# Performance work log

Measured on AMD Instinct MI355X. Metric: run time of the kernel, lower is better.

## Reference

```python
import jax, jax.numpy as jnp
import numpy as np

D_ATT = 256
D_GROUP = 32
N_GROUP = D_ATT // D_GROUP


def setup_inputs() -> dict:
    key = jax.random.key(0)
    ks = jax.random.split(key, 6)
    B, L = 4, 512
    import math
    s = 1.0 / math.sqrt(D_ATT)
    return {
        "x": jax.random.normal(ks[0], (B, L, D_ATT), dtype=jnp.float32),
        "Wq": jax.random.normal(ks[1], (D_ATT, D_ATT), dtype=jnp.float32) * s * 0.06,
        "Wk": jax.random.normal(ks[2], (D_ATT, D_ATT), dtype=jnp.float32) * s * 0.06,
        "Wv": jax.random.normal(ks[3], (D_ATT, D_ATT), dtype=jnp.float32) * s * 0.06,
        "w_mlp": jax.random.normal(ks[4], (D_GROUP,), dtype=jnp.float32) * 0.1,
        "b_mlp": jax.random.normal(ks[5], (1,), dtype=jnp.float32) * 0.1,
    }


def reference(x, Wq, Wk, Wv, w_mlp, b_mlp):
    B, L, d_att = x.shape
    G, Dg = N_GROUP, D_GROUP
    # nn.Linear(bias=False): y = x @ W.T
    Q = x @ Wq.T  # (B, L, d_att)
    K = x @ Wk.T
    V = x @ Wv.T
    Qg = Q.reshape(B, L, 1, G, Dg)
    Kg = K.reshape(B, 1, L, G, Dg)
    # group_MLP: ReLU -> Linear(Dg, 1) -> ReLU, applied to Q-K diff
    # diff: (B, Lq, Lk, G, Dg) -- the huge intermediate a fused kernel would avoid
    diff = Qg - Kg
    attn = jnp.einsum('bqkgd,d->bqkg', jax.nn.relu(diff), w_mlp) + b_mlp[0]
    attn = jax.nn.relu(attn)
    # positional_adding_bias=0, positional_multiplying_bias=1 (defaults), no mask
    attn = jax.nn.softmax(attn, axis=2)  # softmax over key positions
    # NOTE: original views V as (B, L, d_group, n_group) -- asymmetric grouping, kept faithful
    Vg = V.reshape(B, L, Dg, G)
    out = jnp.einsum('bqkg,bkdg->bqdg', attn, Vg)  # (B, Lq, Dg, G)
    return out.reshape(B, L, d_att)
```

## Files before the change

kernel.cpp:

```cpp
#include <hip/hip_runtime.h>

typedef float f32x2 __attribute__((ext_vector_type(2)));
typedef float f32x4 __attribute__((ext_vector_type(4)));
typedef short bf16x8 __attribute__((ext_vector_type(8)));

#define LL 512
#define M_ROWS 2048
#define KC 768

__device__ __forceinline__ float quad_swap1(float x) {
    return __int_as_float(__builtin_amdgcn_mov_dpp(__float_as_int(x), 0xB1, 0xF, 0xF, true));
}
__device__ __forceinline__ float quad_swap2(float x) {
    return __int_as_float(__builtin_amdgcn_mov_dpp(__float_as_int(x), 0x4E, 0xF, 0xF, true));
}

__device__ __forceinline__ unsigned short bf16_rtne(float x) {
    unsigned u = __float_as_uint(x);
    return (unsigned short)((u + 0x7fffu + ((u >> 16) & 1u)) >> 16);
}
__device__ __forceinline__ float bf16_to_f(unsigned short h) {
    return __uint_as_float((unsigned)h << 16);
}

__global__ __launch_bounds__(64) void split_bf16(
    const float* __restrict__ X, const float* __restrict__ Wq,
    const float* __restrict__ Wk, const float* __restrict__ Wv,
    unsigned short* __restrict__ Xc, unsigned short* __restrict__ Wc)
{
    const int row = blockIdx.x;
    const int t = threadIdx.x;
    const float* src;
    unsigned short* hi1; unsigned short* hi2; unsigned short* lo1;
    if (row < M_ROWS) {
        src = X + (size_t)row * 256;
        hi1 = Xc + (size_t)row * KC;
        hi2 = hi1 + 256;
        lo1 = hi1 + 512;
    } else {
        const int n = row - M_ROWS;
        const int mat = n >> 8, c = n & 255;
        const int srow = (mat == 2) ? (((c & 31) << 3) | (c >> 5)) : c;
        src = (mat == 0 ? Wq : (mat == 1 ? Wk : Wv)) + (size_t)srow * 256;
        hi1 = Wc + (size_t)n * KC;
        lo1 = hi1 + 256;
        hi2 = hi1 + 512;
    }
    const f32x4 v = *(const f32x4*)(src + t * 4);
    ushort4 h, l;
    h.x = bf16_rtne(v.x); h.y = bf16_rtne(v.y); h.z = bf16_rtne(v.z); h.w = bf16_rtne(v.w);
    l.x = bf16_rtne(v.x - bf16_to_f(h.x));
    l.y = bf16_rtne(v.y - bf16_to_f(h.y));
    l.z = bf16_rtne(v.z - bf16_to_f(h.z));
    l.w = bf16_rtne(v.w - bf16_to_f(h.w));
    *(ushort4*)(hi1 + t * 4) = h;
    *(ushort4*)(hi2 + t * 4) = h;
    *(ushort4*)(lo1 + t * 4) = l;
}

__global__ __launch_bounds__(64) void qkv_mfma(
    const unsigned short* __restrict__ Xc, const unsigned short* __restrict__ Wc,
    float* __restrict__ Y)
{
    const int bid = blockIdx.x;
    const int m0 = (bid & 31) * 64;
    const int n0 = (bid >> 5) * 64;
    const int l = threadIdx.x;
    const int lr = l & 15;
    const int lk = (l >> 4) * 8;

    size_t aoff[4], boff[4];
#pragma unroll
    for (int i = 0; i < 4; ++i) {
        aoff[i] = (size_t)(m0 + i * 16 + lr) * KC + lk;
        boff[i] = (size_t)(n0 + i * 16 + lr) * KC + lk;
    }

    f32x4 acc[4][4];
#pragma unroll
    for (int i = 0; i < 4; ++i)
#pragma unroll
        for (int j = 0; j < 4; ++j) acc[i][j] = (f32x4){0.f, 0.f, 0.f, 0.f};

    bf16x8 A0[4], B0[4], A1[4], B1[4];
#pragma unroll
    for (int i = 0; i < 4; ++i) {
        A0[i] = *(const bf16x8*)(Xc + aoff[i]);
        B0[i] = *(const bf16x8*)(Wc + boff[i]);
    }

#pragma unroll 1
    for (int it = 0; it < 24; it += 2) {
        const int ks1 = (it + 1) * 32;
#pragma unroll
        for (int i = 0; i < 4; ++i) {
            A1[i] = *(const bf16x8*)(Xc + aoff[i] + ks1);
            B1[i] = *(const bf16x8*)(Wc + boff[i] + ks1);
        }
#pragma unroll
        for (int ai = 0; ai < 4; ++ai)
#pragma unroll
            for (int bi = 0; bi < 4; ++bi)
                acc[ai][bi] = __builtin_amdgcn_mfma_f32_16x16x32_bf16(
                    A0[ai], B0[bi], acc[ai][bi], 0, 0, 0);
        if (it + 2 < 24) {
            const int ks2 = (it + 2) * 32;
#pragma unroll
            for (int i = 0; i < 4; ++i) {
                A0[i] = *(const bf16x8*)(Xc + aoff[i] + ks2);
                B0[i] = *(const bf16x8*)(Wc + boff[i] + ks2);
            }
        }
#pragma unroll
        for (int ai = 0; ai < 4; ++ai)
#pragma unroll
            for (int bi = 0; bi < 4; ++bi)
                acc[ai][bi] = __builtin_amdgcn_mfma_f32_16x16x32_bf16(
                    A1[ai], B1[bi], acc[ai][bi], 0, 0, 0);
    }

    const int mat = n0 >> 8;
    float* Yb = Y + (size_t)mat * M_ROWS * 256;
#pragma unroll
    for (int ai = 0; ai < 4; ++ai)
#pragma unroll
        for (int bi = 0; bi < 4; ++bi) {
            const int col = (n0 & 255) + bi * 16 + lr;
#pragma unroll
            for (int r = 0; r < 4; ++r) {
                const int row = m0 + ai * 16 + (l >> 4) * 4 + r;
                Yb[(size_t)row * 256 + col] = acc[ai][bi][r];
            }
        }
}

#define ACC_S 73
__global__ __launch_bounds__(256, 1) void attn_fused(
    const float* __restrict__ Y,
    const float* __restrict__ w_mlp, const float* __restrict__ b_mlp,
    float* __restrict__ out)
{
    const float* Qm = Y;
    const float* Km = Y + (size_t)M_ROWS * 256;
    const float* Vt = Y + (size_t)2 * M_ROWS * 256;

    const int bid = blockIdx.x;
    const int b = bid & 3;
    const int q0 = (bid >> 2) * 8;

    const int t = threadIdx.x;
    const int dh = t & 3;
    const int g = (t >> 2) & 7;
    const int p = t >> 5;

    __shared__ float accbuf[8][32][ACC_S];
    __shared__ float ltot[8][8];

    const int doff = g * 32 + dh * 8;
    const float bias = b_mlp[0];

    f32x2 w2[4];
    {
        f32x4 wa = *(const f32x4*)(w_mlp + dh * 8);
        f32x4 wb = *(const f32x4*)(w_mlp + dh * 8 + 4);
        w2[0] = __builtin_shufflevector(wa, wa, 0, 1);
        w2[1] = __builtin_shufflevector(wa, wa, 2, 3);
        w2[2] = __builtin_shufflevector(wb, wb, 0, 1);
        w2[3] = __builtin_shufflevector(wb, wb, 2, 3);
    }

    f32x2 qr2[8][4];
#pragma unroll
    for (int q = 0; q < 8; ++q) {
        const float* qp = Qm + ((size_t)(b * LL) + q0 + q) * 256 + doff;
        f32x4 qa = *(const f32x4*)qp;
        f32x4 qb = *(const f32x4*)(qp + 4);
        qr2[q][0] = __builtin_shufflevector(qa, qa, 0, 1);
        qr2[q][1] = __builtin_shufflevector(qa, qa, 2, 3);
        qr2[q][2] = __builtin_shufflevector(qb, qb, 0, 1);
        qr2[q][3] = __builtin_shufflevector(qb, qb, 2, 3);
    }

    f32x2 acc2[8][4];
#pragma unroll
    for (int q = 0; q < 8; ++q)
#pragma unroll
        for (int j = 0; j < 4; ++j) acc2[q][j] = (f32x2){0.f, 0.f};
    float l[8] = {0.f, 0.f, 0.f, 0.f, 0.f, 0.f, 0.f, 0.f};

    const float* kptr = Km + ((size_t)(b * LL) + p) * 256 + doff;
    const float* vptr = Vt + ((size_t)(b * LL) + p) * 256 + doff;

    auto compute = [&](f32x4 ka, f32x4 kb, f32x4 va, f32x4 vb) {
        f32x2 k2[4] = {__builtin_shufflevector(ka, ka, 0, 1),
                       __builtin_shufflevector(ka, ka, 2, 3),
                       __builtin_shufflevector(kb, kb, 0, 1),
                       __builtin_shufflevector(kb, kb, 2, 3)};
        f32x2 v2[4] = {__builtin_shufflevector(va, va, 0, 1),
                       __builtin_shufflevector(va, va, 2, 3),
                       __builtin_shufflevector(vb, vb, 0, 1),
                       __builtin_shufflevector(vb, vb, 2, 3)};
        const f32x2 z2 = {0.f, 0.f};
#pragma unroll
        for (int q = 0; q < 8; ++q) {
            f32x2 s2 = z2;
#pragma unroll
            for (int j = 0; j < 4; ++j) {
                f32x2 d2 = qr2[q][j] - k2[j];
                f32x2 r2 = __builtin_elementwise_max(d2, z2);
                s2 += w2[j] * r2;
            }
            float s = s2.x + s2.y;
            s += quad_swap1(s);
            s += quad_swap2(s);
            s = fmaxf(s + bias, 0.f);
            const float e = __expf(s);
            l[q] += e;
            const f32x2 e2 = {e, e};
#pragma unroll
            for (int j = 0; j < 4; ++j) acc2[q][j] += e2 * v2[j];
        }
    };

    f32x4 ka = *(const f32x4*)kptr, kb = *(const f32x4*)(kptr + 4);
    f32x4 va = *(const f32x4*)vptr, vb = *(const f32x4*)(vptr + 4);
#pragma unroll 1
    for (int i = 0; i < 63; ++i) {
        kptr += 8 * 256; vptr += 8 * 256;
        f32x4 ka2 = *(const f32x4*)kptr, kb2 = *(const f32x4*)(kptr + 4);
        f32x4 va2 = *(const f32x4*)vptr, vb2 = *(const f32x4*)(vptr + 4);
        compute(ka, kb, va, vb);
        ka = ka2; kb = kb2; va = va2; vb = vb2;
    }
    compute(ka, kb, va, vb);

    {
        float* rowp = &accbuf[p][g * 4 + dh][0];
#pragma unroll
        for (int q = 0; q < 8; ++q)
#pragma unroll
            for (int j = 0; j < 4; ++j)
                *(f32x2*)(rowp + q * 8 + j * 2) = acc2[q][j];
        if (dh == 0) {
            float* lp = &accbuf[p][g * 4][64];
#pragma unroll
            for (int q = 0; q < 8; ++q) lp[q] = l[q];
        }
    }
    __syncthreads();

    if (t < 64) {
        const int gg = t >> 3, qq = t & 7;
        float s = 0.f;
#pragma unroll
        for (int pp = 0; pp < 8; ++pp) s += accbuf[pp][gg * 4][64 + qq];
        ltot[gg][qq] = s;
    }
    __syncthreads();

    {
        const int q = t >> 5;
        const int dval = t & 31;
        const int dhh = dval >> 3, jj = dval & 7;
        float res[8];
#pragma unroll
        for (int gg = 0; gg < 8; ++gg) {
            float s = 0.f;
#pragma unroll
            for (int pp = 0; pp < 8; ++pp) s += accbuf[pp][gg * 4 + dhh][q * 8 + jj];
            res[gg] = s / ltot[gg][q];
        }
        float* op = out + ((size_t)(b * LL) + q0 + q) * 256 + dval * 8;
        *(f32x4*)op       = (f32x4){res[0], res[1], res[2], res[3]};
        *(f32x4*)(op + 4) = (f32x4){res[4], res[5], res[6], res[7]};
    }
}

extern "C" void kernel_launch(void* const* d_in, const int* in_sizes, int n_in,
                              void* d_out, int out_size, void* d_ws, size_t ws_size,
                              hipStream_t stream) {
    (void)in_sizes; (void)n_in; (void)out_size; (void)ws_size;
    const float* x     = (const float*)d_in[0];
    const float* Wq    = (const float*)d_in[1];
    const float* Wk    = (const float*)d_in[2];
    const float* Wv    = (const float*)d_in[3];
    const float* w_mlp = (const float*)d_in[4];
    const float* b_mlp = (const float*)d_in[5];
    float* outp = (float*)d_out;

    float* Y = (float*)d_ws;
    unsigned short* Xc = (unsigned short*)((char*)d_ws + (size_t)6291456);
    unsigned short* Wc = (unsigned short*)((char*)d_ws + (size_t)6291456 + 3145728);

    split_bf16<<<dim3(M_ROWS + 768), 64, 0, stream>>>(x, Wq, Wk, Wv, Xc, Wc);
    qkv_mfma<<<dim3(384), 64, 0, stream>>>(Xc, Wc, Y);
    attn_fused<<<dim3(256), 256, 0, stream>>>(Y, w_mlp, b_mlp, outp);
}
```

Measured before the change: 128.8 us.

## Double attention block threads to split keys 16 ways and fold log2e into weights

The attention kernel now launches 512 threads per block instead of 256, so each block splits the key range into 16 partitions of 32 keys rather than 8 of 64. That halves the serial loop length per thread and raises the number of waves per CU. The log2(e) factor is folded into the MLP weights and bias so the kernel can call exp2 directly, and the bias is added as the initial accumulator value. The cross-partition reduction is reworked to run in two halves through a smaller shared buffer, which adds an extra barrier and more LDS reads per output.

```diff
diff --git a/kernel.cpp b/kernel.cpp
--- a/kernel.cpp
+++ b/kernel.cpp
@@ -7,6 +7,13 @@
 #define LL 512
 #define M_ROWS 2048
 #define KC 768
+
+#if __has_builtin(__builtin_amdgcn_exp2f)
+#define EXP2F __builtin_amdgcn_exp2f
+#else
+#define EXP2F exp2f
+#endif
+#define LOG2E 1.44269504088896340736f
 
 __device__ __forceinline__ float quad_swap1(float x) {
     return __int_as_float(__builtin_amdgcn_mov_dpp(__float_as_int(x), 0xB1, 0xF, 0xF, true));
@@ -134,8 +141,7 @@
         }
 }
 
-#define ACC_S 73
-__global__ __launch_bounds__(256, 1) void attn_fused(
+__global__ __launch_bounds__(512, 2) void attn_fused(
     const float* __restrict__ Y,
     const float* __restrict__ w_mlp, const float* __restrict__ b_mlp,
     float* __restrict__ out)
@@ -150,19 +156,20 @@
 
     const int t = threadIdx.x;
     const int dh = t & 3;
-    const int g = (t >> 2) & 7;
     const int p = t >> 5;
-
-    __shared__ float accbuf[8][32][ACC_S];
-    __shared__ float ltot[8][8];
+    const int lane32 = t & 31;
+    const int g = lane32 >> 2;
+
+    __shared__ float accbuf[16][32][37];
 
     const int doff = g * 32 + dh * 8;
-    const float bias = b_mlp[0];
+    const float bias4 = b_mlp[0] * (LOG2E * 0.25f);
 
     f32x2 w2[4];
     {
         f32x4 wa = *(const f32x4*)(w_mlp + dh * 8);
         f32x4 wb = *(const f32x4*)(w_mlp + dh * 8 + 4);
+        wa *= LOG2E; wb *= LOG2E;
         w2[0] = __builtin_shufflevector(wa, wa, 0, 1);
         w2[1] = __builtin_shufflevector(wa, wa, 2, 3);
         w2[2] = __builtin_shufflevector(wb, wb, 0, 1);
@@ -203,7 +210,7 @@
         const f32x2 z2 = {0.f, 0.f};
 #pragma unroll
         for (int q = 0; q < 8; ++q) {
-            f32x2 s2 = z2;
+            f32x2 s2 = {bias4, 0.f};
 #pragma unroll
             for (int j = 0; j < 4; ++j) {
                 f32x2 d2 = qr2[q][j] - k2[j];
@@ -213,8 +220,8 @@
             float s = s2.x + s2.y;
             s += quad_swap1(s);
             s += quad_swap2(s);
-            s = fmaxf(s + bias, 0.f);
-            const float e = __expf(s);
+            s = fmaxf(s, 0.f);
+            const float e = EXP2F(s);
             l[q] += e;
             const f32x2 e2 = {e, e};
 #pragma unroll
@@ -225,8 +232,8 @@
     f32x4 ka = *(const f32x4*)kptr, kb = *(const f32x4*)(kptr + 4);
     f32x4 va = *(const f32x4*)vptr, vb = *(const f32x4*)(vptr + 4);
 #pragma unroll 1
-    for (int i = 0; i < 63; ++i) {
-        kptr += 8 * 256; vptr += 8 * 256;
+    for (int i = 0; i < 31; ++i) {
+        kptr += 16 * 256; vptr += 16 * 256;
         f32x4 ka2 = *(const f32x4*)kptr, kb2 = *(const f32x4*)(kptr + 4);
         f32x4 va2 = *(const f32x4*)vptr, vb2 = *(const f32x4*)(vptr + 4);
         compute(ka, kb, va, vb);
@@ -234,45 +241,61 @@
     }
     compute(ka, kb, va, vb);
 
+    const int c_o = t & 255;
+    const int g_o = c_o & 7, d_o = c_o >> 3;
+    const int rowb = g_o * 4 + (d_o >> 3);
+    const int colb = d_o & 7;
+    const int qsel = t >> 8;
+
     {
-        float* rowp = &accbuf[p][g * 4 + dh][0];
-#pragma unroll
-        for (int q = 0; q < 8; ++q)
+        float* rowp = &accbuf[p][lane32][0];
+#pragma unroll
+        for (int qq = 0; qq < 4; ++qq)
 #pragma unroll
             for (int j = 0; j < 4; ++j)
-                *(f32x2*)(rowp + q * 8 + j * 2) = acc2[q][j];
+                *(f32x2*)(rowp + qq * 8 + j * 2) = acc2[qq][j];
         if (dh == 0) {
-            float* lp = &accbuf[p][g * 4][64];
-#pragma unroll
-            for (int q = 0; q < 8; ++q) lp[q] = l[q];
+#pragma unroll
+            for (int qq = 0; qq < 4; ++qq) accbuf[p][lane32][32 + qq] = l[qq];
         }
     }
     __syncthreads();
-
-    if (t < 64) {
-        const int gg = t >> 3, qq = t & 7;
-        float s = 0.f;
-#pragma unroll
-        for (int pp = 0; pp < 8; ++pp) s += accbuf[pp][gg * 4][64 + qq];
-        ltot[gg][qq] = s;
+#pragma unroll
+    for (int h = 0; h < 2; ++h) {
+        const int qh = qsel + 2 * h;
+        float s = 0.f, ls = 0.f;
+#pragma unroll
+        for (int pp = 0; pp < 16; ++pp) {
+            s  += accbuf[pp][rowb][qh * 8 + colb];
+            ls += accbuf[pp][g_o * 4][32 + qh];
+        }
+        out[((size_t)(b * LL) + q0 + qh) * 256 + c_o] = s / ls;
     }
     __syncthreads();
 
     {
-        const int q = t >> 5;
-        const int dval = t & 31;
-        const int dhh = dval >> 3, jj = dval & 7;
-        float res[8];
-#pragma unroll
-        for (int gg = 0; gg < 8; ++gg) {
-            float s = 0.f;
-#pragma unroll
-            for (int pp = 0; pp < 8; ++pp) s += accbuf[pp][gg * 4 + dhh][q * 8 + jj];
-            res[gg] = s / ltot[gg][q];
-        }
-        float* op = out + ((size_t)(b * LL) + q0 + q) * 256 + dval * 8;
-        *(f32x4*)op       = (f32x4){res[0], res[1], res[2], res[3]};
-        *(f32x4*)(op + 4) = (f32x4){res[4], res[5], res[6], res[7]};
+        float* rowp = &accbuf[p][lane32][0];
+#pragma unroll
+        for (int qq = 0; qq < 4; ++qq)
+#pragma unroll
+            for (int j = 0; j < 4; ++j)
+                *(f32x2*)(rowp + qq * 8 + j * 2) = acc2[4 + qq][j];
+        if (dh == 0) {
+#pragma unroll
+            for (int qq = 0; qq < 4; ++qq) accbuf[p][lane32][32 + qq] = l[4 + qq];
+        }
+    }
+    __syncthreads();
+#pragma unroll
+    for (int h = 0; h < 2; ++h) {
+        const int qh = qsel + 2 * h;
+        float s = 0.f, ls = 0.f;
+#pragma unroll
+        for (int pp = 0; pp < 16; ++pp) {
+            s  += accbuf[pp][rowb][qh * 8 + colb];
+            ls += accbuf[pp][g_o * 4][32 + qh];
+        }
+        out[((size_t)(b * LL) + q0 + 4 + qh) * 256 + c_o] = s / ls;
     }
 }
 
@@ -294,5 +317,5 @@
 
     split_bf16<<<dim3(M_ROWS + 768), 64, 0, stream>>>(x, Wq, Wk, Wv, Xc, Wc);
     qkv_mfma<<<dim3(384), 64, 0, stream>>>(Xc, Wc, Y);
-    attn_fused<<<dim3(256), 256, 0, stream>>>(Y, w_mlp, b_mlp, outp);
-}
+    attn_fused<<<dim3(256), 512, 0, stream>>>(Y, w_mlp, b_mlp, outp);
+}
```

Result: faster. 125.7 us (-2.4%).
